# Kernel tuning notes

Measured on AMD Instinct MI355X. Metric: run time of the kernel, lower is better.

## Reference

```python
import jax, jax.numpy as jnp
import numpy as np

def setup_inputs() -> dict:
    key = jax.random.key(0)
    ks = jax.random.split(key, 8)
    B, C, H, W = 4, 64, 64, 64
    Cr = C // 8
    s = 1.0 / np.sqrt(C)
    return {
        "x": jax.random.normal(ks[0], (B, C, H, W), jnp.float32),
        "wq": jax.random.normal(ks[1], (Cr, C), jnp.float32) * s,
        "bq": jax.random.normal(ks[2], (Cr,), jnp.float32) * 0.01,
        "wk": jax.random.normal(ks[3], (Cr, C), jnp.float32) * s,
        "bk": jax.random.normal(ks[4], (Cr,), jnp.float32) * 0.01,
        "wv": jax.random.normal(ks[5], (C, C), jnp.float32) * s,
        "bv": jax.random.normal(ks[6], (C,), jnp.float32) * 0.01,
        "gamma": jax.random.normal(ks[7], (1,), jnp.float32) * 0.1,
    }

def reference(x, wq, bq, wk, bk, wv, bv, gamma):
    B, C, H, W = x.shape
    N = H * W
    xf = x.reshape(B, C, N)  # 1x1 conv == pointwise linear over channel dim
    q = jnp.einsum("oc,bcn->bno", wq, xf) + bq[None, None, :]   # (B, N, Cr)
    k = jnp.einsum("oc,bcn->bon", wk, xf) + bk[None, :, None]   # (B, Cr, N)
    v = jnp.einsum("oc,bcn->bon", wv, xf) + bv[None, :, None]   # (B, C, N)
    attn = jnp.einsum("bno,bom->bnm", q, k)                     # (B, N, N)
    attn = jax.nn.softmax(attn, axis=-1)
    out = jnp.einsum("bcm,bnm->bcn", v, attn)                   # (B, C, N)
    out = out.reshape(B, C, H, W)
    return x + gamma[0] * out
```

## Files before the change

kernel.cpp:

```cpp
#include <hip/hip_runtime.h>

#define BB 4
#define CC 64
#define NN 4096

typedef __attribute__((ext_vector_type(8)))  short short8;
typedef __attribute__((ext_vector_type(4)))  short short4v;
typedef __attribute__((ext_vector_type(4)))  float f32x4;
typedef __attribute__((ext_vector_type(16))) float f32x16;
typedef unsigned short u16;

#define QWS_ELEMS (BB * NN * 8)

__device__ inline u16 f2bf(float x) {
    unsigned u = __float_as_uint(x);
    u = (u + 0x7fffu + ((u >> 16) & 1u)) >> 16;
    return (u16)u;
}
__device__ inline unsigned pack2rne(float a, float b) {
    return (unsigned)f2bf(a) | ((unsigned)f2bf(b) << 16);
}
__device__ inline unsigned permpack(float lo, float hi) {
    return __builtin_amdgcn_perm(__float_as_uint(hi), __float_as_uint(lo), 0x07060302);
}

union SH8 {
    short8 s;
    struct Halves { short4v lo, hi; } h;
    uint4 u;
};

__global__ __launch_bounds__(256) void proj_kernel(
    const float* __restrict__ x,
    const float* __restrict__ wq, const float* __restrict__ bq,
    const float* __restrict__ wk, const float* __restrict__ bk,
    const float* __restrict__ wv, const float* __restrict__ bv,
    u16* __restrict__ ws_u)
{
    u16* qws = ws_u;
    u16* kws = ws_u + QWS_ELEMS;
    u16* vws = ws_u + 2 * QWS_ELEMS;

    const int y   = blockIdx.y;
    const int pix = blockIdx.x * 256 + threadIdx.x;
    const int b   = pix >> 12;
    const int n   = pix & (NN - 1);
    const float* xb = x + ((size_t)b << 18) + n;

    float xr[CC];
#pragma unroll
    for (int c = 0; c < CC; ++c) xr[c] = xb[(size_t)c << 12];

    if (y <= 1) {
        const float* wp = (y == 0) ? wq : wk;
        const float* bp = (y == 0) ? bq : bk;
        const int v0 = y * 12;
        float a8[8], av[12];
#pragma unroll
        for (int i = 0; i < 8; ++i)  a8[i] = bp[i];
#pragma unroll
        for (int i = 0; i < 12; ++i) av[i] = bv[v0 + i];
#pragma unroll 4
        for (int c = 0; c < CC; ++c) {
            const float xv = xr[c];
#pragma unroll
            for (int i = 0; i < 8; ++i)  a8[i] += wp[i * CC + c] * xv;
#pragma unroll
            for (int i = 0; i < 12; ++i) av[i] += wv[(v0 + i) * CC + c] * xv;
        }
        uint4 p4;
        p4.x = pack2rne(a8[0], a8[1]); p4.y = pack2rne(a8[2], a8[3]);
        p4.z = pack2rne(a8[4], a8[5]); p4.w = pack2rne(a8[6], a8[7]);
        u16* dst = (y == 0) ? qws : kws;
        *(uint4*)&dst[(size_t)pix * 8] = p4;
#pragma unroll
        for (int i = 0; i < 12; ++i)
            vws[(((size_t)((b << 6) + v0 + i)) << 12) + n] = f2bf(av[i]);
    } else {
        const int v0 = 24 + (y - 2) * 20;
        float av[20];
#pragma unroll
        for (int i = 0; i < 20; ++i) av[i] = bv[v0 + i];
#pragma unroll 4
        for (int c = 0; c < CC; ++c) {
            const float xv = xr[c];
#pragma unroll
            for (int i = 0; i < 20; ++i) av[i] += wv[(v0 + i) * CC + c] * xv;
        }
#pragma unroll
        for (int i = 0; i < 20; ++i)
            vws[(((size_t)((b << 6) + v0 + i)) << 12) + n] = f2bf(av[i]);
    }
}

__global__ __launch_bounds__(512) void attn_kernel(
    const float* __restrict__ x, const float* __restrict__ gamma,
    const u16* __restrict__ ws_u, float* __restrict__ out)
{
    const u16* qws = ws_u;
    const u16* kws = ws_u + QWS_ELEMS;
    const u16* vws = ws_u + 2 * QWS_ELEMS;

    __shared__ __align__(16) char smem[34816 + 1024 + 256];
    u16*   v_t    = (u16*)smem;
    float* eb     = (float*)smem;
    float* l_part = (float*)(smem + 34816);
    float* l_inv  = (float*)(smem + 34816 + 1024);

    const int tid  = threadIdx.x;
    const int w    = tid >> 6;
    const int lane = tid & 63;
    const int l31  = lane & 31;
    const int lh   = lane >> 5;
    const int mh   = w >> 1;
    const int qh   = w & 1;

    const int b  = blockIdx.y;
    const int qb = blockIdx.x << 6;
    const int bN = b << 12;

    short8 qf = {0,0,0,0,0,0,0,0};
    short8 kf = {0,0,0,0,0,0,0,0};
    if (lane < 32) {
        qf = *(const short8*)(qws + (size_t)(bN + qb + (qh << 5) + l31) * 8);
        kf = *(const short8*)(kws + (size_t)(bN + (mh << 5) + l31) * 8);
    }

    const int c_st = tid >> 3;
    const int o_st = (tid & 7) << 3;
    const u16* vgr = vws + (((size_t)((b << 6) + c_st)) << 12) + o_st;
    const int st0  = c_st * 132 + o_st;

    SH8 va0, va1, vb0, vb1;
    va0.s = *(const short8*)(vgr);
    va1.s = *(const short8*)(vgr + 64);
    *(short4v*)&v_t[st0]      = va0.h.lo;
    *(short4v*)&v_t[st0 + 4]  = va0.h.hi;
    *(short4v*)&v_t[st0 + 64] = va1.h.lo;
    *(short4v*)&v_t[st0 + 68] = va1.h.hi;
    va0.s = *(const short8*)(vgr + 128);
    va1.s = *(const short8*)(vgr + 192);

    const int rA = l31 * 132;
    const int rB = (32 + l31) * 132;
    const int mb = (mh << 5) + (lh << 2);

    f32x16 z16, acc0, acc1;
#pragma unroll
    for (int r = 0; r < 16; ++r) { z16[r] = 0.f; acc0[r] = 0.f; acc1[r] = 0.f; }
    float ls = 0.f;

    __syncthreads();

#pragma unroll 2
    for (int it = 0; it < 32; ++it) {
        const int buf = (it & 1) * (CC * 132);
        const int nxt = ((it + 1) & 31) << 7;
        const int nx2 = ((it + 2) & 31) << 7;

        f32x16 d = __builtin_amdgcn_mfma_f32_32x32x16_bf16(kf, qf, z16, 0, 0, 0);

        if (lane < 32)
            kf = *(const short8*)(kws + (size_t)(bN + nxt + (mh << 5) + l31) * 8);
        vb0.s = *(const short8*)(vgr + nx2);
        vb1.s = *(const short8*)(vgr + nx2 + 64);

        float p[16];
#pragma unroll
        for (int r = 0; r < 16; ++r) p[r] = __expf(d[r]);
        float s0 = 0.f, s1 = 0.f;
#pragma unroll
        for (int r = 0; r < 8; ++r) { s0 += p[2 * r]; s1 += p[2 * r + 1]; }
        ls += s0 + s1;

        SH8 A0, A1;
        A0.u.x = permpack(p[0],  p[1]);  A0.u.y = permpack(p[2],  p[3]);
        A0.u.z = permpack(p[4],  p[5]);  A0.u.w = permpack(p[6],  p[7]);
        A1.u.x = permpack(p[8],  p[9]);  A1.u.y = permpack(p[10], p[11]);
        A1.u.z = permpack(p[12], p[13]); A1.u.w = permpack(p[14], p[15]);

        SH8 B00, B01, B10, B11;
        B00.h.lo = *(const short4v*)&v_t[buf + rA + mb];
        B00.h.hi = *(const short4v*)&v_t[buf + rA + mb + 8];
        B01.h.lo = *(const short4v*)&v_t[buf + rB + mb];
        B01.h.hi = *(const short4v*)&v_t[buf + rB + mb + 8];
        B10.h.lo = *(const short4v*)&v_t[buf + rA + mb + 16];
        B10.h.hi = *(const short4v*)&v_t[buf + rA + mb + 24];
        B11.h.lo = *(const short4v*)&v_t[buf + rB + mb + 16];
        B11.h.hi = *(const short4v*)&v_t[buf + rB + mb + 24];

        acc0 = __builtin_amdgcn_mfma_f32_32x32x16_bf16(A0.s, B00.s, acc0, 0, 0, 0);
        acc1 = __builtin_amdgcn_mfma_f32_32x32x16_bf16(A0.s, B01.s, acc1, 0, 0, 0);
        acc0 = __builtin_amdgcn_mfma_f32_32x32x16_bf16(A1.s, B10.s, acc0, 0, 0, 0);
        acc1 = __builtin_amdgcn_mfma_f32_32x32x16_bf16(A1.s, B11.s, acc1, 0, 0, 0);

        const int ob = (CC * 132) - buf;
        *(short4v*)&v_t[ob + st0]      = va0.h.lo;
        *(short4v*)&v_t[ob + st0 + 4]  = va0.h.hi;
        *(short4v*)&v_t[ob + st0 + 64] = va1.h.lo;
        *(short4v*)&v_t[ob + st0 + 68] = va1.h.hi;
        va0 = vb0; va1 = vb1;

        __syncthreads();
    }

    float lt = ls + __shfl_xor(ls, 32, 64);
    if (lane < 32) l_part[(mh * 2 + qh) * 32 + l31] = lt;
    __syncthreads();
    if (w < 2 && lane < 32) {
        float s = l_part[(0 * 2 + qh) * 32 + l31] + l_part[(1 * 2 + qh) * 32 + l31]
                + l_part[(2 * 2 + qh) * 32 + l31] + l_part[(3 * 2 + qh) * 32 + l31];
        l_inv[qh * 32 + l31] = 1.0f / s;
    }

    if (mh >= 2) {
        float* e0 = &eb[(((mh - 2) << 2) + (qh << 1) + 0) * 1088 + lane * 17];
        float* e1 = &eb[(((mh - 2) << 2) + (qh << 1) + 1) * 1088 + lane * 17];
#pragma unroll
        for (int r = 0; r < 16; ++r) { e0[r] = acc0[r]; e1[r] = acc1[r]; }
    }
    __syncthreads();
    if (mh < 2) {
        const float* e0 = &eb[((mh << 2) + (qh << 1) + 0) * 1088 + lane * 17];
        const float* e1 = &eb[((mh << 2) + (qh << 1) + 1) * 1088 + lane * 17];
#pragma unroll
        for (int r = 0; r < 16; ++r) { acc0[r] += e0[r]; acc1[r] += e1[r]; }
    }
    __syncthreads();
    if (mh == 1) {
        float* e0 = &eb[((qh << 1) + 0) * 1088 + lane * 17];
        float* e1 = &eb[((qh << 1) + 1) * 1088 + lane * 17];
#pragma unroll
        for (int r = 0; r < 16; ++r) { e0[r] = acc0[r]; e1[r] = acc1[r]; }
    }
    __syncthreads();
    if (w < 2) {
        const float* e0 = &eb[((qh << 1) + 0) * 1088 + lane * 17];
        const float* e1 = &eb[((qh << 1) + 1) * 1088 + lane * 17];
#pragma unroll
        for (int r = 0; r < 16; ++r) { acc0[r] += e0[r]; acc1[r] += e1[r]; }

        f32x4 li[4];
#pragma unroll
        for (int k = 0; k < 4; ++k)
            li[k] = *(const f32x4*)&l_inv[qh * 32 + (k << 3) + (lh << 2)];
        const float g = gamma[0];
#pragma unroll
        for (int ch = 0; ch < 2; ++ch) {
            const int c = (ch << 5) + l31;
            const f32x16 a = ch ? acc1 : acc0;
            const size_t rowb = (((size_t)((b << 6) + c)) << 12) + qb + (qh << 5);
#pragma unroll
            for (int k = 0; k < 4; ++k) {
                const int q0 = (k << 3) + (lh << 2);
                const float4 xv = *(const float4*)&x[rowb + q0];
                float4 o;
                o.x = xv.x + g * a[4 * k + 0] * li[k][0];
                o.y = xv.y + g * a[4 * k + 1] * li[k][1];
                o.z = xv.z + g * a[4 * k + 2] * li[k][2];
                o.w = xv.w + g * a[4 * k + 3] * li[k][3];
                *(float4*)&out[rowb + q0] = o;
            }
        }
    }
}

extern "C" void kernel_launch(void* const* d_in, const int* in_sizes, int n_in,
                              void* d_out, int out_size, void* d_ws, size_t ws_size,
                              hipStream_t stream)
{
    const float* x     = (const float*)d_in[0];
    const float* wq    = (const float*)d_in[1];
    const float* bq    = (const float*)d_in[2];
    const float* wk    = (const float*)d_in[3];
    const float* bk    = (const float*)d_in[4];
    const float* wv    = (const float*)d_in[5];
    const float* bv    = (const float*)d_in[6];
    const float* gamma = (const float*)d_in[7];
    u16*   ws  = (u16*)d_ws;
    float* out = (float*)d_out;

    hipLaunchKernelGGL(proj_kernel, dim3(BB * NN / 256, 4), dim3(256), 0, stream,
                       x, wq, bq, wk, bk, wv, bv, ws);
    hipLaunchKernelGGL(attn_kernel, dim3(NN / 64, BB), dim3(512), 0, stream,
                       x, gamma, ws, out);
}
```

Measured before the change: 106.8 us.

## Split projection into 9 channel-group slices and use lgkm-only barriers in attention

The projection kernel now uses 512-thread blocks and a 9-way y split: eight slices each compute 8 V channels, and one slice computes both Q and K. x is streamed per channel rather than held as 64 registers. This is meant to cut register pressure and spread the V work more evenly. In the attention loop, the next K fragment is loaded into a separate register before the score MFMA, and __syncthreads is replaced by an inline-asm s_waitcnt lgkmcnt(0) plus s_barrier, so outstanding global (vmcnt) loads need not drain at each barrier. The cost is that x is now read from global memory 9 times instead of 4, and the hand-written barrier depends on the compiler keeping the memory ordering correct.

```diff
diff --git a/kernel.cpp b/kernel.cpp
--- a/kernel.cpp
+++ b/kernel.cpp
@@ -24,13 +24,17 @@
     return __builtin_amdgcn_perm(__float_as_uint(hi), __float_as_uint(lo), 0x07060302);
 }
 
+__device__ inline void barrier_lgkm() {
+    asm volatile("s_waitcnt lgkmcnt(0)\n\ts_barrier" ::: "memory");
+}
+
 union SH8 {
     short8 s;
     struct Halves { short4v lo, hi; } h;
     uint4 u;
 };
 
-__global__ __launch_bounds__(256) void proj_kernel(
+__global__ __launch_bounds__(512) void proj_kernel(
     const float* __restrict__ x,
     const float* __restrict__ wq, const float* __restrict__ bq,
     const float* __restrict__ wk, const float* __restrict__ bk,
@@ -42,54 +46,46 @@
     u16* vws = ws_u + 2 * QWS_ELEMS;
 
     const int y   = blockIdx.y;
-    const int pix = blockIdx.x * 256 + threadIdx.x;
+    const int pix = blockIdx.x * 512 + threadIdx.x;
     const int b   = pix >> 12;
     const int n   = pix & (NN - 1);
     const float* xb = x + ((size_t)b << 18) + n;
 
-    float xr[CC];
-#pragma unroll
-    for (int c = 0; c < CC; ++c) xr[c] = xb[(size_t)c << 12];
-
-    if (y <= 1) {
-        const float* wp = (y == 0) ? wq : wk;
-        const float* bp = (y == 0) ? bq : bk;
-        const int v0 = y * 12;
-        float a8[8], av[12];
-#pragma unroll
-        for (int i = 0; i < 8; ++i)  a8[i] = bp[i];
-#pragma unroll
-        for (int i = 0; i < 12; ++i) av[i] = bv[v0 + i];
-#pragma unroll 4
+    if (y < 8) {
+        const int v0 = y << 3;
+        float av[8];
+#pragma unroll
+        for (int i = 0; i < 8; ++i) av[i] = bv[v0 + i];
+#pragma unroll 8
         for (int c = 0; c < CC; ++c) {
-            const float xv = xr[c];
-#pragma unroll
-            for (int i = 0; i < 8; ++i)  a8[i] += wp[i * CC + c] * xv;
-#pragma unroll
-            for (int i = 0; i < 12; ++i) av[i] += wv[(v0 + i) * CC + c] * xv;
+            const float xv = xb[(size_t)c << 12];
+#pragma unroll
+            for (int i = 0; i < 8; ++i)
+                av[i] += wv[(v0 + i) * CC + c] * xv;
         }
-        uint4 p4;
-        p4.x = pack2rne(a8[0], a8[1]); p4.y = pack2rne(a8[2], a8[3]);
-        p4.z = pack2rne(a8[4], a8[5]); p4.w = pack2rne(a8[6], a8[7]);
-        u16* dst = (y == 0) ? qws : kws;
-        *(uint4*)&dst[(size_t)pix * 8] = p4;
-#pragma unroll
-        for (int i = 0; i < 12; ++i)
+#pragma unroll
+        for (int i = 0; i < 8; ++i)
             vws[(((size_t)((b << 6) + v0 + i)) << 12) + n] = f2bf(av[i]);
     } else {
-        const int v0 = 24 + (y - 2) * 20;
-        float av[20];
-#pragma unroll
-        for (int i = 0; i < 20; ++i) av[i] = bv[v0 + i];
-#pragma unroll 4
+        float aq[8], ak[8];
+#pragma unroll
+        for (int i = 0; i < 8; ++i) { aq[i] = bq[i]; ak[i] = bk[i]; }
+#pragma unroll 8
         for (int c = 0; c < CC; ++c) {
-            const float xv = xr[c];
-#pragma unroll
-            for (int i = 0; i < 20; ++i) av[i] += wv[(v0 + i) * CC + c] * xv;
+            const float xv = xb[(size_t)c << 12];
+#pragma unroll
+            for (int i = 0; i < 8; ++i) {
+                aq[i] += wq[i * CC + c] * xv;
+                ak[i] += wk[i * CC + c] * xv;
+            }
         }
-#pragma unroll
-        for (int i = 0; i < 20; ++i)
-            vws[(((size_t)((b << 6) + v0 + i)) << 12) + n] = f2bf(av[i]);
+        uint4 qp, kp;
+        qp.x = pack2rne(aq[0], aq[1]); qp.y = pack2rne(aq[2], aq[3]);
+        qp.z = pack2rne(aq[4], aq[5]); qp.w = pack2rne(aq[6], aq[7]);
+        kp.x = pack2rne(ak[0], ak[1]); kp.y = pack2rne(ak[2], ak[3]);
+        kp.z = pack2rne(ak[4], ak[5]); kp.w = pack2rne(ak[6], ak[7]);
+        *(uint4*)&qws[(size_t)pix * 8] = qp;
+        *(uint4*)&kws[(size_t)pix * 8] = kp;
     }
 }
 
@@ -125,6 +121,7 @@
         qf = *(const short8*)(qws + (size_t)(bN + qb + (qh << 5) + l31) * 8);
         kf = *(const short8*)(kws + (size_t)(bN + (mh << 5) + l31) * 8);
     }
+    short8 kn = kf;
 
     const int c_st = tid >> 3;
     const int o_st = (tid & 7) << 3;
@@ -150,7 +147,7 @@
     for (int r = 0; r < 16; ++r) { z16[r] = 0.f; acc0[r] = 0.f; acc1[r] = 0.f; }
     float ls = 0.f;
 
-    __syncthreads();
+    barrier_lgkm();
 
 #pragma unroll 2
     for (int it = 0; it < 32; ++it) {
@@ -158,12 +155,12 @@
         const int nxt = ((it + 1) & 31) << 7;
         const int nx2 = ((it + 2) & 31) << 7;
 
-        f32x16 d = __builtin_amdgcn_mfma_f32_32x32x16_bf16(kf, qf, z16, 0, 0, 0);
-
-        if (lane < 32)
-            kf = *(const short8*)(kws + (size_t)(bN + nxt + (mh << 5) + l31) * 8);
         vb0.s = *(const short8*)(vgr + nx2);
         vb1.s = *(const short8*)(vgr + nx2 + 64);
+        if (lane < 32)
+            kn = *(const short8*)(kws + (size_t)(bN + nxt + (mh << 5) + l31) * 8);
+
+        f32x16 d = __builtin_amdgcn_mfma_f32_32x32x16_bf16(kf, qf, z16, 0, 0, 0);
 
         float p[16];
 #pragma unroll
@@ -200,8 +197,9 @@
         *(short4v*)&v_t[ob + st0 + 64] = va1.h.lo;
         *(short4v*)&v_t[ob + st0 + 68] = va1.h.hi;
         va0 = vb0; va1 = vb1;
-
-        __syncthreads();
+        kf = kn;
+
+        barrier_lgkm();
     }
 
     float lt = ls + __shfl_xor(ls, 32, 64);
@@ -280,7 +278,7 @@
     u16*   ws  = (u16*)d_ws;
     float* out = (float*)d_out;
 
-    hipLaunchKernelGGL(proj_kernel, dim3(BB * NN / 256, 4), dim3(256), 0, stream,
+    hipLaunchKernelGGL(proj_kernel, dim3(BB * NN / 512, 9), dim3(512), 0, stream,
                        x, wq, bq, wk, bk, wv, bv, ws);
     hipLaunchKernelGGL(attn_kernel, dim3(NN / 64, BB), dim3(512), 0, stream,
                        x, gamma, ws, out);
```

Result: no change. 105.9 us (-0.8%).
